# Performance work log

Measured on AMD Instinct MI355X. Metric: run time of the kernel, lower is better.

The kernel has to match this reference:

```python
import jax, jax.numpy as jnp
import numpy as np

HIDDEN = 128
NUM_TYPES = 13
LN_EPS = 1e-5


def setup_inputs() -> dict:
    key = jax.random.key(0)
    k_adj, k_emb, k_idx, k_w, k_b = jax.random.split(key, 5)
    B, N, M, H, T = 8, 4096, 2048, HIDDEN, NUM_TYPES
    adj = jax.random.uniform(k_adj, (B, N, M), dtype=jnp.float32)
    embeds = jax.random.normal(k_emb, (B, N, H), dtype=jnp.float32)
    node_type_index = jax.random.randint(k_idx, (B, N), 0, T, dtype=jnp.int32)
    node_mask = jnp.ones((B, N), dtype=bool)
    # per-type Linear params (nn.Linear default init ~ U(-1/sqrt(H), 1/sqrt(H)))
    lim = 1.0 / np.sqrt(H)
    W = jax.random.uniform(k_w, (T, H, H), dtype=jnp.float32, minval=-lim, maxval=lim)
    b = jax.random.uniform(k_b, (T, H), dtype=jnp.float32, minval=-lim, maxval=lim)
    gamma = jnp.ones((H,), dtype=jnp.float32)
    beta = jnp.zeros((H,), dtype=jnp.float32)
    return {"adj": adj, "embeds": embeds, "node_type_index": node_type_index,
            "node_mask": node_mask, "W": W, "b": b, "gamma": gamma, "beta": beta}


def reference(adj, embeds, node_type_index, node_mask, W, b, gamma, beta):
    T = W.shape[0]
    # per-node-type linear: compute all T projections, then route by type.
    # y: [T, B, N, H]
    y = jnp.einsum('bnh,thd->tbnd', embeds, W) + b[:, None, None, :]
    onehot = jax.nn.one_hot(node_type_index, T, dtype=embeds.dtype)  # [B, N, T]
    routed = jnp.einsum('tbnd,bnt->bnd', y, onehot)                   # [B, N, H]
    x = jnp.where(node_mask[..., None], routed, embeds)
    # LayerNorm over hidden dim
    mu = jnp.mean(x, axis=-1, keepdims=True)
    var = jnp.mean(jnp.square(x - mu), axis=-1, keepdims=True)
    x = (x - mu) * jax.lax.rsqrt(var + LN_EPS) * gamma + beta
    # two-stage hypergraph aggregation: adj^T @ x, then adj @ lat
    lat = jnp.einsum('bnm,bnh->bmh', adj, x)   # [B, M, H]
    ret = jnp.einsum('bnm,bmh->bnh', adj, lat)  # [B, N, H]
    return ret
```

## Files before the change

kernel.cpp:

```cpp
#include <hip/hip_runtime.h>
#include <stdint.h>
#include <stddef.h>


typedef float    f32x4_t  __attribute__((ext_vector_type(4)));
typedef __bf16   bf16x8_t __attribute__((ext_vector_type(8)));
typedef unsigned int u32x4_t __attribute__((ext_vector_type(4)));
typedef unsigned int u32x2_t __attribute__((ext_vector_type(2)));

__device__ __forceinline__ unsigned short f2bf(float f) {
    union { float f; unsigned int u; } v; v.f = f;
    unsigned int u = v.u;
    return (unsigned short)((u + 0x7FFFu + ((u >> 16) & 1u)) >> 16);
}

__device__ __forceinline__ unsigned int cvtpk(float a, float b) {
    unsigned int r;
    asm("v_cvt_pk_bf16_f32 %0, %1, %2" : "=v"(r) : "v"(a), "v"(b));
    return r;
}

__device__ __forceinline__ bool mask_on(const unsigned char* m, int gid) {
    return (m[gid] | m[(gid >> 2) << 2]) != 0;
}

__device__ __forceinline__ int foff(int row, int g) {
    return row * 128 + (((g) ^ (row & 7)) << 4);
}

template<int GSTRIDE>
__device__ __forceinline__ void stage_B(const unsigned short* __restrict__ gb,
                                        int k0, unsigned short* ldsB, int t)
{
    const int l = t & 63, w = t >> 6;
    const int hsub = l >> 3;
    const int csrc = ((l & 7) ^ hsub) << 3;
    #pragma unroll
    for (int i = 0; i < 4; ++i) {
        const int hbase = i * 32 + w * 8;
        const unsigned short* src = gb + (size_t)(hbase + hsub) * GSTRIDE + k0 + csrc;
        unsigned short* dst = ldsB + hbase * 64;
        __builtin_amdgcn_global_load_lds(
            (__attribute__((address_space(1))) void*)src,
            (__attribute__((address_space(3))) void*)dst, 16, 0, 0);
    }
}

__device__ __forceinline__ void stage_A3(const unsigned short* __restrict__ ab,
                                         int k0, unsigned short* ldsA, int t)
{
    const int l = t & 63, w = t >> 6;
    const int rsub = l >> 3;
    const int csrc = ((l & 7) ^ rsub) << 3;
    const unsigned short* src = ab + (size_t)(w * 8 + rsub) * 2048 + k0 + csrc;
    unsigned short* dst = ldsA + (w * 8) * 64;
    __builtin_amdgcn_global_load_lds(
        (__attribute__((address_space(1))) void*)src,
        (__attribute__((address_space(3))) void*)dst, 16, 0, 0);
}

__global__ __launch_bounds__(256) void k0_wtrans(
    const float* __restrict__ W, unsigned short* __restrict__ WT)
{
    __shared__ float tile[128][132];
    const int t = threadIdx.x, ty = blockIdx.x;
    const float* Wt = W + (size_t)ty * 128 * 128;
    for (int it = 0; it < 16; ++it) {
        int idx = it * 256 + t;
        int h = idx >> 5, c = (idx & 31) * 4;
        *(float4*)(&tile[h][c]) = *(const float4*)(Wt + h * 128 + c);
    }
    __syncthreads();
    const int d = t >> 1, half = t & 1, h0 = half * 64;
    unsigned short* out = WT + ((size_t)ty * 128 + d) * 128 + h0;
    #pragma unroll
    for (int ch = 0; ch < 8; ++ch) {
        int h = h0 + ch * 8;
        u32x4_t o;
        o[0] = cvtpk(tile[h + 0][d], tile[h + 1][d]);
        o[1] = cvtpk(tile[h + 2][d], tile[h + 3][d]);
        o[2] = cvtpk(tile[h + 4][d], tile[h + 5][d]);
        o[3] = cvtpk(tile[h + 6][d], tile[h + 7][d]);
        *(u32x4_t*)(out + ch * 8) = o;
    }
}

__global__ __launch_bounds__(256) void k1_typed_ln(
    const float* __restrict__ embeds,
    const int*   __restrict__ ntype,
    const unsigned char* __restrict__ mask8,
    const unsigned short* __restrict__ WT,
    const float* __restrict__ bias,
    const float* __restrict__ gamma,
    const float* __restrict__ beta,
    unsigned short* __restrict__ xT)
{
    __shared__ unsigned short e_lds[64][136];
    __shared__ unsigned short y_lds[64][136];
    __shared__ unsigned short lists[13][64];
    __shared__ int cnt[13];
    __shared__ int grp_ty[32], grp_base[32], grp_n;
    __shared__ unsigned char msk[64];
    __shared__ float g_lds[128], be_lds[128];

    const int t   = threadIdx.x;
    const int bid = blockIdx.x;
    const int b   = bid & 7;
    const int n0  = (bid >> 3) << 6;
    const int gbase = b * 4096 + n0;
    const float* ebase = embeds + (size_t)gbase * 128;

    {
        const int n = t >> 2, q = t & 3;
        const float* src = ebase + n * 128 + q * 32;
        #pragma unroll
        for (int c = 0; c < 4; ++c) {
            f32x4_t va = *(const f32x4_t*)(src + c * 8);
            f32x4_t vb = *(const f32x4_t*)(src + c * 8 + 4);
            u32x4_t o;
            o[0] = cvtpk(va[0], va[1]); o[1] = cvtpk(va[2], va[3]);
            o[2] = cvtpk(vb[0], vb[1]); o[3] = cvtpk(vb[2], vb[3]);
            *(u32x4_t*)(&e_lds[n][q * 32 + c * 8]) = o;
        }
    }
    if (t < 128) { g_lds[t] = gamma[t]; be_lds[t] = beta[t]; }
    if (t < 64)  msk[t] = mask_on(mask8, gbase + t) ? 1 : 0;
    if (t < 13)  cnt[t] = 0;
    __syncthreads();

    if (t < 64) {
        int ty = ntype[(size_t)gbase + t];
        int slot = atomicAdd(&cnt[ty], 1);
        lists[ty][slot] = (unsigned short)t;
    }
    __syncthreads();
    if (t == 0) {
        int g = 0;
        for (int ty = 0; ty < 13; ++ty) {
            int c = cnt[ty];
            for (int base = 0; base < c; base += 16) {
                grp_ty[g] = ty; grp_base[g] = base; ++g;
            }
        }
        grp_n = g;
    }
    __syncthreads();

    const int NG   = grp_n;
    const int lane = t & 63, wv = t >> 6;
    const int fr = lane & 15, fg = lane >> 4;
    const int d0 = wv * 32;

    for (int g = 0; g < NG; ++g) {
        const int ty = grp_ty[g], base = grp_base[g];
        const int cend = cnt[ty] - 1;
        const int nodeA = lists[ty][min(base + fr, cend)];

        bf16x8_t afr[4];
        #pragma unroll
        for (int kk = 0; kk < 4; ++kk)
            afr[kk] = __builtin_bit_cast(bf16x8_t,
                *(const u32x4_t*)(&e_lds[nodeA][kk * 32 + fg * 8]));

        const unsigned short* wt = WT + (size_t)ty * 128 * 128;
        f32x4_t acc0 = f32x4_t{0.f, 0.f, 0.f, 0.f};
        f32x4_t acc1 = f32x4_t{0.f, 0.f, 0.f, 0.f};
        #pragma unroll
        for (int kk = 0; kk < 4; ++kk) {
            bf16x8_t b0 = __builtin_bit_cast(bf16x8_t,
                *(const u32x4_t*)(wt + (size_t)(d0 + fr) * 128 + kk * 32 + fg * 8));
            bf16x8_t b1 = __builtin_bit_cast(bf16x8_t,
                *(const u32x4_t*)(wt + (size_t)(d0 + 16 + fr) * 128 + kk * 32 + fg * 8));
            acc0 = __builtin_amdgcn_mfma_f32_16x16x32_bf16(afr[kk], b0, acc0, 0, 0, 0);
            acc1 = __builtin_amdgcn_mfma_f32_16x16x32_bf16(afr[kk], b1, acc1, 0, 0, 0);
        }

        const float bs0 = bias[ty * 128 + d0 + fr];
        const float bs1 = bias[ty * 128 + d0 + 16 + fr];
        #pragma unroll
        for (int j = 0; j < 4; ++j) {
            const int nd = lists[ty][min(base + fg * 4 + j, cend)];
            if (msk[nd]) {
                y_lds[nd][d0 + fr]      = f2bf(acc0[j] + bs0);
                y_lds[nd][d0 + 16 + fr] = f2bf(acc1[j] + bs1);
            } else {
                y_lds[nd][d0 + fr]      = e_lds[nd][d0 + fr];
                y_lds[nd][d0 + 16 + fr] = e_lds[nd][d0 + 16 + fr];
            }
        }
    }
    __syncthreads();

    for (int i = 0; i < 16; ++i) {
        const int n = wv + i * 4;
        unsigned int u = *(const unsigned int*)(&y_lds[n][lane * 2]);
        float vx = __builtin_bit_cast(float, u << 16);
        float vy = __builtin_bit_cast(float, u & 0xffff0000u);
        float s = vx + vy;
        float q = vx * vx + vy * vy;
        #pragma unroll
        for (int mw = 32; mw >= 1; mw >>= 1) {
            s += __shfl_xor(s, mw);
            q += __shfl_xor(q, mw);
        }
        const float mu  = s * 0.0078125f;
        const float var = q * 0.0078125f - mu * mu;
        const float r   = rsqrtf(var + 1e-5f);
        const float ox = (vx - mu) * r * g_lds[lane * 2]     + be_lds[lane * 2];
        const float oy = (vy - mu) * r * g_lds[lane * 2 + 1] + be_lds[lane * 2 + 1];
        *(unsigned int*)(&y_lds[n][lane * 2]) = cvtpk(ox, oy);
    }
    __syncthreads();

    const int nl = t & 63, hg = t >> 6;
    unsigned short* xrow = xT + (size_t)b * 128 * 4096 + n0 + nl;
    for (int i = 0; i < 32; ++i) {
        const int h = hg * 32 + i;
        xrow[(size_t)h * 4096] = y_lds[nl][h];
    }
}

__global__ __launch_bounds__(256) void k2_lat(
    const float* __restrict__ adj,
    const unsigned short* __restrict__ xT,
    unsigned short* __restrict__ latT,
    unsigned short* __restrict__ adjbf)
{
    __shared__ unsigned short Al[2][32 * 64];
    __shared__ unsigned short Bl[2][128 * 64];

    const int t   = threadIdx.x;
    const int bid = blockIdx.x;
    const int b   = bid & 7;
    const int m0  = (bid >> 3) << 5;
    const float* adjb = adj + (size_t)b * 4096 * 2048;
    const unsigned short* xb = xT + (size_t)b * 128 * 4096;
    unsigned short* abf = adjbf + (size_t)b * 4096 * 2048;

    const int lane = t & 63, wv = t >> 6;
    const int wm = wv & 1, wh = wv >> 1;

    const int a_kp = t >> 3;
    const int a_m  = (t & 7) << 2;

    const int fr = lane & 15, fg = lane >> 4;
    int offA[2], offB[4][2];
    #pragma unroll
    for (int kk = 0; kk < 2; ++kk) offA[kk] = foff(wm * 16 + fr, kk * 4 + fg);
    #pragma unroll
    for (int j = 0; j < 4; ++j)
        #pragma unroll
        for (int kk = 0; kk < 2; ++kk)
            offB[j][kk] = foff(wh * 64 + j * 16 + fr, kk * 4 + fg);

    f32x4_t ar0, ar1;
    auto LOAD_A = [&](int k0) {
        const float* p = adjb + (size_t)(k0 + a_kp * 2) * 2048 + m0 + a_m;
        ar0 = *(const f32x4_t*)(p);
        ar1 = *(const f32x4_t*)(p + 2048);
    };
    auto WRITE_A = [&](int buf, int k0) {
        const int g = a_kp >> 2, wrd = a_kp & 3;
        #pragma unroll
        for (int j = 0; j < 4; ++j) {
            const int m = a_m + j;
            unsigned int pk = cvtpk(ar0[j], ar1[j]);
            *(unsigned int*)((char*)(&Al[buf][0]) + m * 128 + ((g ^ (m & 7)) << 4) + wrd * 4) = pk;
        }
        const size_t row = (size_t)(k0 + a_kp * 2);
        u32x2_t r0, r1;
        r0[0] = cvtpk(ar0[0], ar0[1]); r0[1] = cvtpk(ar0[2], ar0[3]);
        r1[0] = cvtpk(ar1[0], ar1[1]); r1[1] = cvtpk(ar1[2], ar1[3]);
        *(u32x2_t*)(abf + row * 2048 + m0 + a_m) = r0;
        *(u32x2_t*)(abf + (row + 1) * 2048 + m0 + a_m) = r1;
    };

    f32x4_t acc[4];
    #pragma unroll
    for (int j = 0; j < 4; ++j) acc[j] = f32x4_t{0.f, 0.f, 0.f, 0.f};

    LOAD_A(0);
    stage_B<4096>(xb, 0, &Bl[0][0], t);
    WRITE_A(0, 0);
    __syncthreads();

    for (int s = 0; s < 64; ++s) {
        const int buf = s & 1;
        if (s < 63) {
            LOAD_A((s + 1) * 64);
            stage_B<4096>(xb, (s + 1) * 64, &Bl[buf ^ 1][0], t);
        }
        bf16x8_t af[2];
        #pragma unroll
        for (int kk = 0; kk < 2; ++kk)
            af[kk] = __builtin_bit_cast(bf16x8_t,
                *(const u32x4_t*)((const char*)(&Al[buf][0]) + offA[kk]));
        #pragma unroll
        for (int j = 0; j < 4; ++j) {
            #pragma unroll
            for (int kk = 0; kk < 2; ++kk) {
                bf16x8_t bfj = __builtin_bit_cast(bf16x8_t,
                    *(const u32x4_t*)((const char*)(&Bl[buf][0]) + offB[j][kk]));
                acc[j] = __builtin_amdgcn_mfma_f32_16x16x32_bf16(af[kk], bfj, acc[j], 0, 0, 0);
            }
        }
        if (s < 63) WRITE_A(buf ^ 1, (s + 1) * 64);
        __syncthreads();
    }

    const int mrow = m0 + wm * 16 + (lane >> 4) * 4;
    #pragma unroll
    for (int j = 0; j < 4; ++j) {
        int col = wh * 64 + j * 16 + fr;
        unsigned int o0 = cvtpk(acc[j][0], acc[j][1]);
        unsigned int o1 = cvtpk(acc[j][2], acc[j][3]);
        unsigned int* dst = (unsigned int*)(latT + (size_t)(b * 128 + col) * 2048 + mrow);
        dst[0] = o0; dst[1] = o1;
    }
}

__global__ __launch_bounds__(256) void k3_ret(
    const unsigned short* __restrict__ adjbf,
    const unsigned short* __restrict__ latT,
    float* __restrict__ ret)
{
    __shared__ unsigned short Al[2][32 * 64];
    __shared__ unsigned short Bl[2][128 * 64];

    const int t   = threadIdx.x;
    const int bid = blockIdx.x;
    const int b   = bid & 7;
    const int n0  = (bid >> 3) << 5;
    const unsigned short* ab = adjbf + (size_t)b * 4096 * 2048 + (size_t)n0 * 2048;
    const unsigned short* lb = latT + (size_t)b * 128 * 2048;

    const int lane = t & 63, wv = t >> 6;
    const int wn = wv & 1, wh = wv >> 1;

    const int fr = lane & 15, fg = lane >> 4;
    int offA[2], offB[4][2];
    #pragma unroll
    for (int kk = 0; kk < 2; ++kk) offA[kk] = foff(wn * 16 + fr, kk * 4 + fg);
    #pragma unroll
    for (int j = 0; j < 4; ++j)
        #pragma unroll
        for (int kk = 0; kk < 2; ++kk)
            offB[j][kk] = foff(wh * 64 + j * 16 + fr, kk * 4 + fg);

    f32x4_t acc[4];
    #pragma unroll
    for (int j = 0; j < 4; ++j) acc[j] = f32x4_t{0.f, 0.f, 0.f, 0.f};

    stage_A3(ab, 0, &Al[0][0], t);
    stage_B<2048>(lb, 0, &Bl[0][0], t);
    __syncthreads();

    for (int s = 0; s < 32; ++s) {
        const int buf = s & 1;
        if (s < 31) {
            stage_A3(ab, (s + 1) * 64, &Al[buf ^ 1][0], t);
            stage_B<2048>(lb, (s + 1) * 64, &Bl[buf ^ 1][0], t);
        }
        bf16x8_t af[2];
        #pragma unroll
        for (int kk = 0; kk < 2; ++kk)
            af[kk] = __builtin_bit_cast(bf16x8_t,
                *(const u32x4_t*)((const char*)(&Al[buf][0]) + offA[kk]));
        #pragma unroll
        for (int j = 0; j < 4; ++j) {
            #pragma unroll
            for (int kk = 0; kk < 2; ++kk) {
                bf16x8_t bfj = __builtin_bit_cast(bf16x8_t,
                    *(const u32x4_t*)((const char*)(&Bl[buf][0]) + offB[j][kk]));
                acc[j] = __builtin_amdgcn_mfma_f32_16x16x32_bf16(af[kk], bfj, acc[j], 0, 0, 0);
            }
        }
        __syncthreads();
    }

    const int nrow = n0 + wn * 16 + (lane >> 4) * 4;
    #pragma unroll
    for (int j = 0; j < 4; ++j) {
        int col = wh * 64 + j * 16 + fr;
        #pragma unroll
        for (int jj = 0; jj < 4; ++jj) {
            ret[((size_t)b * 4096 + nrow + jj) * 128 + col] = acc[j][jj];
        }
    }
}

extern "C" void kernel_launch(void* const* d_in, const int* in_sizes, int n_in,
                              void* d_out, int out_size, void* d_ws, size_t ws_size,
                              hipStream_t stream) {
    const float* adj    = (const float*)d_in[0];
    const float* embeds = (const float*)d_in[1];
    const int*   ntype  = (const int*)d_in[2];
    const unsigned char* mask8 = (const unsigned char*)d_in[3];
    const float* W      = (const float*)d_in[4];
    const float* bias   = (const float*)d_in[5];
    const float* gamma  = (const float*)d_in[6];
    const float* beta   = (const float*)d_in[7];
    float* ret = (float*)d_out;

    unsigned short* xT    = (unsigned short*)d_ws;
    unsigned short* latT  = xT + (size_t)8 * 128 * 4096;
    unsigned short* WT    = latT + (size_t)8 * 128 * 2048;
    unsigned short* adjbf = WT + (size_t)13 * 128 * 128;

    hipLaunchKernelGGL(k0_wtrans, dim3(13), dim3(256), 0, stream, W, WT);
    hipLaunchKernelGGL(k1_typed_ln, dim3(512), dim3(256), 0, stream,
                       embeds, ntype, mask8, WT, bias, gamma, beta, xT);
    hipLaunchKernelGGL(k2_lat, dim3(512), dim3(256), 0, stream, adj, xT, latT, adjbf);
    hipLaunchKernelGGL(k3_ret, dim3(1024), dim3(256), 0, stream, adjbf, latT, ret);
}
```

Before: 192.0 us.

## Split adj fp32-to-bf16 conversion into a separate streaming kernel

Adds a grid-stride kernel that converts the full fp32 adjacency to bf16 with nontemporal loads before the other kernels run. The latent GEMM then reads bf16 adjacency and builds its LDS tiles with byte permutes instead of converting and writing the bf16 copy itself. This takes conversion and extra global stores out of the GEMM's inner loop, but adds a full extra read of the bf16 adjacency and one more kernel launch.

```diff
diff --git a/kernel.cpp b/kernel.cpp
--- a/kernel.cpp
+++ b/kernel.cpp
@@ -57,6 +57,21 @@
     __builtin_amdgcn_global_load_lds(
         (__attribute__((address_space(1))) void*)src,
         (__attribute__((address_space(3))) void*)dst, 16, 0, 0);
+}
+
+__global__ __launch_bounds__(256) void k_conv(
+    const float* __restrict__ adj, unsigned short* __restrict__ adjbf)
+{
+    const size_t total = (size_t)8 * 4096 * 2048;
+    const size_t stride = (size_t)gridDim.x * 256 * 8;
+    for (size_t i = ((size_t)blockIdx.x * 256 + threadIdx.x) * 8; i < total; i += stride) {
+        f32x4_t a = __builtin_nontemporal_load((const f32x4_t*)(adj + i));
+        f32x4_t b = __builtin_nontemporal_load((const f32x4_t*)(adj + i + 4));
+        u32x4_t o;
+        o[0] = cvtpk(a[0], a[1]); o[1] = cvtpk(a[2], a[3]);
+        o[2] = cvtpk(b[0], b[1]); o[3] = cvtpk(b[2], b[3]);
+        *(u32x4_t*)(adjbf + i) = o;
+    }
 }
 
 __global__ __launch_bounds__(256) void k0_wtrans(
@@ -221,10 +236,9 @@
 }
 
 __global__ __launch_bounds__(256) void k2_lat(
-    const float* __restrict__ adj,
+    const unsigned short* __restrict__ adjbf,
     const unsigned short* __restrict__ xT,
-    unsigned short* __restrict__ latT,
-    unsigned short* __restrict__ adjbf)
+    unsigned short* __restrict__ latT)
 {
     __shared__ unsigned short Al[2][32 * 64];
     __shared__ unsigned short Bl[2][128 * 64];
@@ -233,9 +247,8 @@
     const int bid = blockIdx.x;
     const int b   = bid & 7;
     const int m0  = (bid >> 3) << 5;
-    const float* adjb = adj + (size_t)b * 4096 * 2048;
+    const unsigned short* ab = adjbf + (size_t)b * 4096 * 2048;
     const unsigned short* xb = xT + (size_t)b * 128 * 4096;
-    unsigned short* abf = adjbf + (size_t)b * 4096 * 2048;
 
     const int lane = t & 63, wv = t >> 6;
     const int wm = wv & 1, wh = wv >> 1;
@@ -253,26 +266,24 @@
         for (int kk = 0; kk < 2; ++kk)
             offB[j][kk] = foff(wh * 64 + j * 16 + fr, kk * 4 + fg);
 
-    f32x4_t ar0, ar1;
+    u32x2_t ar0, ar1;
     auto LOAD_A = [&](int k0) {
-        const float* p = adjb + (size_t)(k0 + a_kp * 2) * 2048 + m0 + a_m;
-        ar0 = *(const f32x4_t*)(p);
-        ar1 = *(const f32x4_t*)(p + 2048);
+        const unsigned short* p = ab + (size_t)(k0 + a_kp * 2) * 2048 + m0 + a_m;
+        ar0 = *(const u32x2_t*)(p);
+        ar1 = *(const u32x2_t*)(p + 2048);
     };
-    auto WRITE_A = [&](int buf, int k0) {
+    auto WRITE_A = [&](int buf) {
         const int g = a_kp >> 2, wrd = a_kp & 3;
+        unsigned int pk[4];
+        pk[0] = __builtin_amdgcn_perm(ar1[0], ar0[0], 0x05040100u);
+        pk[1] = __builtin_amdgcn_perm(ar1[0], ar0[0], 0x07060302u);
+        pk[2] = __builtin_amdgcn_perm(ar1[1], ar0[1], 0x05040100u);
+        pk[3] = __builtin_amdgcn_perm(ar1[1], ar0[1], 0x07060302u);
         #pragma unroll
         for (int j = 0; j < 4; ++j) {
             const int m = a_m + j;
-            unsigned int pk = cvtpk(ar0[j], ar1[j]);
-            *(unsigned int*)((char*)(&Al[buf][0]) + m * 128 + ((g ^ (m & 7)) << 4) + wrd * 4) = pk;
-        }
-        const size_t row = (size_t)(k0 + a_kp * 2);
-        u32x2_t r0, r1;
-        r0[0] = cvtpk(ar0[0], ar0[1]); r0[1] = cvtpk(ar0[2], ar0[3]);
-        r1[0] = cvtpk(ar1[0], ar1[1]); r1[1] = cvtpk(ar1[2], ar1[3]);
-        *(u32x2_t*)(abf + row * 2048 + m0 + a_m) = r0;
-        *(u32x2_t*)(abf + (row + 1) * 2048 + m0 + a_m) = r1;
+            *(unsigned int*)((char*)(&Al[buf][0]) + m * 128 + ((g ^ (m & 7)) << 4) + wrd * 4) = pk[j];
+        }
     };
 
     f32x4_t acc[4];
@@ -281,7 +292,7 @@
 
     LOAD_A(0);
     stage_B<4096>(xb, 0, &Bl[0][0], t);
-    WRITE_A(0, 0);
+    WRITE_A(0);
     __syncthreads();
 
     for (int s = 0; s < 64; ++s) {
@@ -304,7 +315,7 @@
                 acc[j] = __builtin_amdgcn_mfma_f32_16x16x32_bf16(af[kk], bfj, acc[j], 0, 0, 0);
             }
         }
-        if (s < 63) WRITE_A(buf ^ 1, (s + 1) * 64);
+        if (s < 63) WRITE_A(buf ^ 1);
         __syncthreads();
     }
 
@@ -407,9 +418,10 @@
     unsigned short* WT    = latT + (size_t)8 * 128 * 2048;
     unsigned short* adjbf = WT + (size_t)13 * 128 * 128;
 
+    hipLaunchKernelGGL(k_conv, dim3(2048), dim3(256), 0, stream, adj, adjbf);
     hipLaunchKernelGGL(k0_wtrans, dim3(13), dim3(256), 0, stream, W, WT);
     hipLaunchKernelGGL(k1_typed_ln, dim3(512), dim3(256), 0, stream,
                        embeds, ntype, mask8, WT, bias, gamma, beta, xT);
-    hipLaunchKernelGGL(k2_lat, dim3(512), dim3(256), 0, stream, adj, xT, latT, adjbf);
+    hipLaunchKernelGGL(k2_lat, dim3(512), dim3(256), 0, stream, adjbf, xT, latT);
     hipLaunchKernelGGL(k3_ret, dim3(1024), dim3(256), 0, stream, adjbf, latT, ret);
 }
```

Result: slower. 200.0 us (+4.2%).
